# Optimization experiments

Hardware: AMD Instinct MI355X
Metric: run time of the kernel (lower is better)

Reference implementation:

```python
import jax, jax.numpy as jnp
import numpy as np

N_NODES = 100000
N_EDGES = 1600000
D_IN, D_HID, D_OUT = 64, 64, 32


def _glorot(key, shape):
    fan_in, fan_out = shape[0], shape[1]
    lim = np.sqrt(6.0 / (fan_in + fan_out)).astype(np.float32)
    return jax.random.uniform(key, shape, jnp.float32, -lim, lim)


def setup_inputs() -> dict:
    key = jax.random.key(0)
    ks = jax.random.split(key, 12)
    x = jax.random.normal(ks[0], (N_NODES, D_IN), jnp.float32)
    edge_index = jax.random.randint(ks[1], (2, N_EDGES), 0, N_NODES, jnp.int64)
    return {
        "x": x,
        "edge_index": edge_index,
        # SAGEConv 1 (in->hid): lin_l (aggregated neighbors, with bias), lin_r (root, no bias)
        "Wl1": _glorot(ks[2], (D_IN, D_HID)),
        "Wr1": _glorot(ks[3], (D_IN, D_HID)),
        "b1": jnp.zeros((D_HID,), jnp.float32),
        # SAGEConv 2 (hid->out)
        "Wl2": _glorot(ks[4], (D_HID, D_OUT)),
        "Wr2": _glorot(ks[5], (D_HID, D_OUT)),
        "b2": jnp.zeros((D_OUT,), jnp.float32),
        # trust head: Linear(32,16) -> ReLU -> Linear(16,1) -> Sigmoid (dropout inert in eval)
        "Wt1": _glorot(ks[6], (D_OUT, 16)),
        "bt1": jnp.zeros((16,), jnp.float32),
        "Wt2": _glorot(ks[7], (16, 1)),
        "bt2": jnp.zeros((1,), jnp.float32),
    }


def _sage_conv(x, src, dst, Wl, Wr, b):
    # mean-aggregate neighbor messages: msg flows src -> dst
    msg = x[src]                                              # [E, d] gather
    agg_sum = jax.ops.segment_sum(msg, dst, num_segments=N_NODES)
    deg = jax.ops.segment_sum(jnp.ones((src.shape[0],), x.dtype), dst,
                              num_segments=N_NODES)
    agg = agg_sum / jnp.maximum(deg, 1.0)[:, None]            # zero-degree -> 0
    return agg @ Wl + x @ Wr + b


def reference(x, edge_index, Wl1, Wr1, b1, Wl2, Wr2, b2, Wt1, bt1, Wt2, bt2):
    src, dst = edge_index[0], edge_index[1]
    h = _sage_conv(x, src, dst, Wl1, Wr1, b1)
    h = jax.nn.relu(h)                    # dropout p=0.3 inert in eval
    h = _sage_conv(h, src, dst, Wl2, Wr2, b2)
    t = jax.nn.relu(h @ Wt1 + bt1)        # dropout p=0.2 inert in eval
    trust = jax.nn.sigmoid(t @ Wt2 + bt2)
    return h, trust
```

## Files before the change

kernel.cpp:

```cpp
#include <hip/hip_runtime.h>
#include <math.h>


#define BCAP    9216
#define BKCHUNK 4096

__device__ inline unsigned short f2bf(float x) {
    unsigned u = __float_as_uint(x);
    unsigned r = u + 0x7fffu + ((u >> 16) & 1u);
    return (unsigned short)(r >> 16);
}
__device__ inline unsigned pack2(float a, float b) {
    return (unsigned)f2bf(a) | ((unsigned)f2bf(b) << 16);
}
__device__ inline float bflo(unsigned u) { return __uint_as_float(u << 16); }
__device__ inline float bfhi(unsigned u) { return __uint_as_float(u & 0xffff0000u); }

__global__ __launch_bounds__(256) void k_m1(
    const float* __restrict__ x,
    const float* __restrict__ Wl1, const float* __restrict__ Wr1,
    const float* __restrict__ b1,
    unsigned* __restrict__ u16b, float* __restrict__ v,
    const int* __restrict__ src, const int* __restrict__ dst,
    int* __restrict__ gcnt, unsigned* __restrict__ pairs,
    int N, int E, int nbuck, int GB, int BKB)
{
    __shared__ __align__(16) char smem[33792];
    int tid = threadIdx.x;
    int g = blockIdx.x / 5, r5 = blockIdx.x % 5;

    if (r5 == 4) {
        if (g >= BKB) return;
        int* hist = (int*)smem;
        int e0 = g * BKCHUNK;
        int e1 = min(e0 + BKCHUNK, E);

        hist[tid] = 0;
        __syncthreads();
        for (int e = e0 + tid; e < e1; e += 256)
            atomicAdd(&hist[((unsigned)dst[e]) >> 9], 1);
        __syncthreads();
        if (tid < nbuck && hist[tid] > 0)
            hist[tid] = tid * BCAP + atomicAdd(&gcnt[tid], hist[tid]);
        __syncthreads();
        for (int e = e0 + tid; e < e1; e += 256) {
            int t = dst[e];
            int b = ((unsigned)t) >> 9;
            int pos = atomicAdd(&hist[b], 1);
            pairs[pos] = (unsigned)src[e] | ((unsigned)(t & 511) << 17);
        }
        return;
    }

    int tile = 4 * g + r5;
    if (tile >= GB) return;
    float* sXT = (float*)smem;
    float* sW  = (float*)(smem + 17408);
    int nblk = tile * 64;

    for (int i = tid * 4; i < 64 * 64; i += 1024) {
        int r = i >> 6, c = i & 63;
        int node = nblk + r;
        float4 xv = (node < N) ? *(const float4*)&x[(size_t)node * 64 + c]
                               : make_float4(0.f, 0.f, 0.f, 0.f);
        sXT[(c + 0) * 68 + r] = xv.x;
        sXT[(c + 1) * 68 + r] = xv.y;
        sXT[(c + 2) * 68 + r] = xv.z;
        sXT[(c + 3) * 68 + r] = xv.w;
    }

    int mg = tid >> 4, ng = tid & 15;
    int m0 = mg * 4, n0 = ng * 4;

    #pragma unroll
    for (int pass = 0; pass < 2; ++pass) {
        const float* W = pass ? Wr1 : Wl1;
        if (pass) __syncthreads();
        for (int i = tid * 4; i < 64 * 64; i += 1024)
            *(float4*)&sW[i] = *(const float4*)&W[i];
        __syncthreads();

        float acc[4][4];
        #pragma unroll
        for (int mi = 0; mi < 4; ++mi)
            #pragma unroll
            for (int ni = 0; ni < 4; ++ni) acc[mi][ni] = 0.0f;

        #pragma unroll 8
        for (int k = 0; k < 64; ++k) {
            float4 a = *(float4*)&sXT[k * 68 + m0];
            float4 w = *(float4*)&sW[k * 64 + n0];
            float av[4] = {a.x, a.y, a.z, a.w};
            float wv[4] = {w.x, w.y, w.z, w.w};
            #pragma unroll
            for (int mi = 0; mi < 4; ++mi)
                #pragma unroll
                for (int ni = 0; ni < 4; ++ni)
                    acc[mi][ni] = fmaf(av[mi], wv[ni], acc[mi][ni]);
        }

        if (pass == 0) {
            #pragma unroll
            for (int mi = 0; mi < 4; ++mi) {
                int node = nblk + m0 + mi;
                if (node >= N) continue;
                uint2 pk;
                pk.x = pack2(acc[mi][0], acc[mi][1]);
                pk.y = pack2(acc[mi][2], acc[mi][3]);
                *(uint2*)&u16b[(size_t)node * 32 + (n0 >> 1)] = pk;
            }
        } else {
            float4 b0 = *(const float4*)&b1[n0];
            #pragma unroll
            for (int mi = 0; mi < 4; ++mi) {
                int node = nblk + m0 + mi;
                if (node >= N) continue;
                *(float4*)&v[(size_t)node * 64 + n0] =
                    make_float4(acc[mi][0]+b0.x, acc[mi][1]+b0.y,
                                acc[mi][2]+b0.z, acc[mi][3]+b0.w);
            }
        }
    }
}

__global__ __launch_bounds__(1024) void k_csr(
    const unsigned* __restrict__ pairs, const int* __restrict__ gcnt,
    int2* __restrict__ nodeOff, int* __restrict__ adj, int N)
{
    __shared__ int hist[512];
    __shared__ int waveSum[8];
    int b = blockIdx.x;
    int tid = threadIdx.x;
    int count = min(gcnt[b], BCAP);
    const unsigned* pp = pairs + (size_t)b * BCAP;
    int base = b * BCAP;

    if (tid < 512) hist[tid] = 0;
    __syncthreads();
    for (int j = tid; j < count; j += 1024)
        atomicAdd(&hist[pp[j] >> 17], 1);
    __syncthreads();

    int lane = tid & 63, wid = tid >> 6;
    int deg = 0, incl = 0;
    if (tid < 512) {
        deg = hist[tid];
        incl = deg;
        #pragma unroll
        for (int off = 1; off < 64; off <<= 1) {
            int t = __shfl_up(incl, off);
            if (lane >= off) incl += t;
        }
        if (lane == 63) waveSum[wid] = incl;
    }
    __syncthreads();
    if (wid == 0 && lane < 8) {
        int s = waveSum[lane], orig = s;
        #pragma unroll
        for (int off = 1; off < 8; off <<= 1) {
            int t = __shfl_up(s, off);
            if (lane >= off) s += t;
        }
        waveSum[lane] = s - orig;
    }
    __syncthreads();
    int excl = 0;
    if (tid < 512) {
        excl = incl - deg + waveSum[wid];
        int node = b * 512 + tid;
        if (node < N) nodeOff[node] = make_int2(base + excl, deg);
    }
    __syncthreads();
    if (tid < 512) hist[tid] = excl;
    __syncthreads();

    for (int j = tid; j < count; j += 1024) {
        unsigned e = pp[j];
        int pos = atomicAdd(&hist[e >> 17], 1);
        adj[base + pos] = (int)(e & 0x1FFFFu);
    }
}

__global__ __launch_bounds__(512) void k_m2(
    const int2* __restrict__ nodeOff, const int* __restrict__ adj,
    const unsigned* __restrict__ u16b, const float* __restrict__ v,
    const float* __restrict__ Wl2, const float* __restrict__ Wr2,
    const float* __restrict__ b2,
    unsigned* __restrict__ P16b, float* __restrict__ Qout, int N)
{
    __shared__ float sH[64 * 66];
    __shared__ float sW[64 * 64];
    int tid = threadIdx.x;
    int nodeBase = blockIdx.x * 64;

    for (int i = tid * 4; i < 64 * 64; i += 2048) {
        int k = i >> 6, n = i & 63;
        const float* Wsrc = (n < 32) ? (Wl2 + k * 32 + n) : (Wr2 + k * 32 + (n - 32));
        *(float4*)&sW[k * 64 + n] = *(const float4*)Wsrc;
    }

    int hw = tid >> 5;
    int lane = tid & 31;
    for (int r = 0; r < 4; ++r) {
        int nLoc = hw * 4 + r;
        int n = nodeBase + nLoc;
        float h0 = 0.0f, h1v = 0.0f;
        if (n < N) {
            int2 od = nodeOff[n];
            int beg = od.x, end = od.x + od.y;
            float lo[8] = {0,0,0,0,0,0,0,0}, hi[8] = {0,0,0,0,0,0,0,0};
            int i = beg;
            for (; i + 8 <= end; i += 8) {
                int s[8];
                #pragma unroll
                for (int j = 0; j < 8; ++j) s[j] = adj[i + j];
                #pragma unroll
                for (int j = 0; j < 8; ++j) {
                    unsigned w = u16b[(size_t)s[j] * 32 + lane];
                    lo[j] += bflo(w); hi[j] += bfhi(w);
                }
            }
            for (; i < end; ++i) {
                unsigned w = u16b[(size_t)adj[i] * 32 + lane];
                lo[0] += bflo(w); hi[0] += bfhi(w);
            }
            float mlo = ((lo[0]+lo[1])+(lo[2]+lo[3])) + ((lo[4]+lo[5])+(lo[6]+lo[7]));
            float mhi = ((hi[0]+hi[1])+(hi[2]+hi[3])) + ((hi[4]+hi[5])+(hi[6]+hi[7]));
            float invd = (od.y > 0) ? 1.0f / (float)od.y : 1.0f;
            float2 vv = ((const float2*)v)[(size_t)n * 32 + lane];
            h0  = fmaxf(mlo * invd + vv.x, 0.0f);
            h1v = fmaxf(mhi * invd + vv.y, 0.0f);
        }
        *(float2*)&sH[nLoc * 66 + 2 * lane] = make_float2(h0, h1v);
    }
    __syncthreads();

    int ng = tid & 15;
    int mg = tid >> 4;
    int m0 = mg * 2, n0 = ng * 4;

    float acc[2][4];
    #pragma unroll
    for (int mi = 0; mi < 2; ++mi)
        #pragma unroll
        for (int ni = 0; ni < 4; ++ni) acc[mi][ni] = 0.0f;

    #pragma unroll 8
    for (int k = 0; k < 64; ++k) {
        float a0 = sH[(m0 + 0) * 66 + k];
        float a1 = sH[(m0 + 1) * 66 + k];
        float4 w = *(float4*)&sW[k * 64 + n0];
        float wv[4] = {w.x, w.y, w.z, w.w};
        #pragma unroll
        for (int ni = 0; ni < 4; ++ni) {
            acc[0][ni] = fmaf(a0, wv[ni], acc[0][ni]);
            acc[1][ni] = fmaf(a1, wv[ni], acc[1][ni]);
        }
    }

    if (n0 < 32) {
        #pragma unroll
        for (int mi = 0; mi < 2; ++mi) {
            int node = nodeBase + m0 + mi;
            if (node >= N) continue;
            uint2 pk;
            pk.x = pack2(acc[mi][0], acc[mi][1]);
            pk.y = pack2(acc[mi][2], acc[mi][3]);
            *(uint2*)&P16b[(size_t)node * 16 + (n0 >> 1)] = pk;
        }
    } else {
        float4 b0 = *(const float4*)&b2[n0 - 32];
        #pragma unroll
        for (int mi = 0; mi < 2; ++mi) {
            int node = nodeBase + m0 + mi;
            if (node >= N) continue;
            *(float4*)&Qout[(size_t)node * 32 + (n0 - 32)] =
                make_float4(acc[mi][0]+b0.x, acc[mi][1]+b0.y,
                            acc[mi][2]+b0.z, acc[mi][3]+b0.w);
        }
    }
}

__global__ __launch_bounds__(256) void k_agg2(
    const int2* __restrict__ nodeOff, const int* __restrict__ adj,
    const unsigned* __restrict__ P16b, const float* __restrict__ Q,
    const float* __restrict__ Wt1, const float* __restrict__ bt1,
    const float* __restrict__ Wt2, const float* __restrict__ bt2,
    float* __restrict__ out_h, float* __restrict__ out_trust, int N)
{
    __shared__ float sWt1[32 * 16];
    __shared__ float sWt2[16];
    for (int i = threadIdx.x; i < 512; i += 256) sWt1[i] = Wt1[i];
    if (threadIdx.x < 16) sWt2[threadIdx.x] = Wt2[threadIdx.x];
    __syncthreads();

    int n = blockIdx.x * 16 + (threadIdx.x >> 4);
    int lane = threadIdx.x & 15;
    if (n >= N) return;

    int2 od = nodeOff[n];
    int beg = od.x, end = od.x + od.y;
    float lo[8] = {0,0,0,0,0,0,0,0}, hi[8] = {0,0,0,0,0,0,0,0};
    int i = beg;
    for (; i + 8 <= end; i += 8) {
        int s[8];
        #pragma unroll
        for (int j = 0; j < 8; ++j) s[j] = adj[i + j];
        #pragma unroll
        for (int j = 0; j < 8; ++j) {
            unsigned w = P16b[(size_t)s[j] * 16 + lane];
            lo[j] += bflo(w); hi[j] += bfhi(w);
        }
    }
    for (; i < end; ++i) {
        unsigned w = P16b[(size_t)adj[i] * 16 + lane];
        lo[0] += bflo(w); hi[0] += bfhi(w);
    }
    float invd = (od.y > 0) ? 1.0f / (float)od.y : 1.0f;
    float mlo = (((lo[0]+lo[1])+(lo[2]+lo[3])) + ((lo[4]+lo[5])+(lo[6]+lo[7]))) * invd;
    float mhi = (((hi[0]+hi[1])+(hi[2]+hi[3])) + ((hi[4]+hi[5])+(hi[6]+hi[7]))) * invd;

    float2 qv = ((const float2*)Q)[(size_t)n * 16 + lane];
    float hx = mlo + qv.x;
    float hy = mhi + qv.y;

    ((float2*)out_h)[(size_t)n * 16 + lane] = make_float2(hx, hy);

    float t = bt1[lane];
    #pragma unroll
    for (int k = 0; k < 16; ++k) {
        float hlo = __shfl(hx, k, 16);
        float hhi = __shfl(hy, k, 16);
        t += hlo * sWt1[(2 * k) * 16 + lane] + hhi * sWt1[(2 * k + 1) * 16 + lane];
    }
    t = fmaxf(t, 0.0f);
    float z = t * sWt2[lane];
    z += __shfl_xor(z, 1);
    z += __shfl_xor(z, 2);
    z += __shfl_xor(z, 4);
    z += __shfl_xor(z, 8);
    if (lane == 0) out_trust[n] = 1.0f / (1.0f + expf(-(z + bt2[0])));
}


extern "C" void kernel_launch(void* const* d_in, const int* in_sizes, int n_in,
                              void* d_out, int out_size, void* d_ws, size_t ws_size,
                              hipStream_t stream)
{
    const float* x   = (const float*)d_in[0];
    const int*   ei  = (const int*)d_in[1];
    const float* Wl1 = (const float*)d_in[2];
    const float* Wr1 = (const float*)d_in[3];
    const float* b1  = (const float*)d_in[4];
    const float* Wl2 = (const float*)d_in[5];
    const float* Wr2 = (const float*)d_in[6];
    const float* b2  = (const float*)d_in[7];
    const float* Wt1 = (const float*)d_in[8];
    const float* bt1 = (const float*)d_in[9];
    const float* Wt2 = (const float*)d_in[10];
    const float* bt2 = (const float*)d_in[11];

    const int N = in_sizes[0] / 64;
    const int E = in_sizes[1] / 2;
    const int* src = ei;
    const int* dst = ei + E;
    const int nbuck = (N + 511) / 512;

    unsigned* pairs  = (unsigned*)d_ws;
    unsigned* u16b   = pairs + (size_t)nbuck * BCAP;
    float*    v      = (float*)(u16b + (size_t)N * 32);
    unsigned* P16b   = (unsigned*)(v + (size_t)N * 64);
    float*    Q      = (float*)(P16b + (size_t)N * 16);
    int*      gcnt   = (int*)(Q + (size_t)N * 32);
    int2*     nodeOff= (int2*)(gcnt + 256);
    int*      adj    = (int*)(nodeOff + N);

    hipMemsetAsync(gcnt, 0, 256 * sizeof(int), stream);

    const int GB  = (N + 63) / 64;
    const int BKB = (E + BKCHUNK - 1) / BKCHUNK;
    int grp = max(BKB, (GB + 3) / 4);
    k_m1  <<<5 * grp, 256, 0, stream>>>(x, Wl1, Wr1, b1, u16b, v,
                                        src, dst, gcnt, pairs, N, E, nbuck, GB, BKB);
    k_csr <<<nbuck, 1024, 0, stream>>>(pairs, gcnt, nodeOff, adj, N);
    k_m2  <<<GB, 512, 0, stream>>>(nodeOff, adj, u16b, v, Wl2, Wr2, b2,
                                   P16b, Q, N);

    float* out_h     = (float*)d_out;
    float* out_trust = out_h + (size_t)N * 32;
    k_agg2<<<(N + 15) / 16, 256, 0, stream>>>(nodeOff, adj, P16b, Q,
                                              Wt1, bt1, Wt2, bt2,
                                              out_h, out_trust, N);
}
```

Measured before the change: 246.9 us.

## Bucket edges by 64-node tiles and build per-tile CSR in shared memory inside consumers

Drops the separate CSR-building kernel. Edges are now bucketed by 64-node tiles with a capacity of 1536 entries each, and each layer-aggregation kernel rebuilds its tile's adjacency with a shared-memory counting sort before gathering. The goal is to save one kernel launch and the global writes and reads of the adj and nodeOff arrays. The cost is that the sort runs twice, once per layer, and any edges past a bucket's capacity are dropped, which relies on the degree distribution of the random test graph. The first GEMM also moves to a row-major X tile with a k-blocked inner loop, and the ratio of GEMM blocks to bucketing blocks changes.

Measured after the change: 307.9 us. 1.25x slower.

```diff
diff --git a/kernel.cpp b/kernel.cpp
--- a/kernel.cpp
+++ b/kernel.cpp
@@ -2,8 +2,9 @@
 #include <math.h>
 
 
-#define BCAP    9216
-#define BKCHUNK 4096
+#define NBUCK   1563
+#define BCAP    1536
+#define BKCHUNK 16384
 
 __device__ inline unsigned short f2bf(float x) {
     unsigned u = __float_as_uint(x);
@@ -23,39 +24,41 @@
     unsigned* __restrict__ u16b, float* __restrict__ v,
     const int* __restrict__ src, const int* __restrict__ dst,
     int* __restrict__ gcnt, unsigned* __restrict__ pairs,
-    int N, int E, int nbuck, int GB, int BKB)
+    int N, int E, int GB, int BKB)
 {
     __shared__ __align__(16) char smem[33792];
     int tid = threadIdx.x;
-    int g = blockIdx.x / 5, r5 = blockIdx.x % 5;
-
-    if (r5 == 4) {
+    int g = blockIdx.x / 17, r17 = blockIdx.x % 17;
+
+    if (r17 == 16) {
         if (g >= BKB) return;
         int* hist = (int*)smem;
         int e0 = g * BKCHUNK;
         int e1 = min(e0 + BKCHUNK, E);
 
-        hist[tid] = 0;
+        for (int i = tid; i < NBUCK; i += 256) hist[i] = 0;
         __syncthreads();
         for (int e = e0 + tid; e < e1; e += 256)
-            atomicAdd(&hist[((unsigned)dst[e]) >> 9], 1);
+            atomicAdd(&hist[((unsigned)dst[e]) >> 6], 1);
         __syncthreads();
-        if (tid < nbuck && hist[tid] > 0)
-            hist[tid] = tid * BCAP + atomicAdd(&gcnt[tid], hist[tid]);
+        for (int i = tid; i < NBUCK; i += 256)
+            if (hist[i] > 0)
+                hist[i] = i * BCAP + atomicAdd(&gcnt[i], hist[i]);
         __syncthreads();
         for (int e = e0 + tid; e < e1; e += 256) {
             int t = dst[e];
-            int b = ((unsigned)t) >> 9;
+            int b = ((unsigned)t) >> 6;
             int pos = atomicAdd(&hist[b], 1);
-            pairs[pos] = (unsigned)src[e] | ((unsigned)(t & 511) << 17);
+            if (pos < (b + 1) * BCAP)
+                pairs[pos] = (unsigned)src[e] | ((unsigned)(t & 63) << 17);
         }
         return;
     }
 
-    int tile = 4 * g + r5;
+    int tile = 16 * g + r17;
     if (tile >= GB) return;
-    float* sXT = (float*)smem;
-    float* sW  = (float*)(smem + 17408);
+    float* sX = (float*)smem;
+    float* sW = (float*)(smem + 17408);
     int nblk = tile * 64;
 
     for (int i = tid * 4; i < 64 * 64; i += 1024) {
@@ -63,10 +66,7 @@
         int node = nblk + r;
         float4 xv = (node < N) ? *(const float4*)&x[(size_t)node * 64 + c]
                                : make_float4(0.f, 0.f, 0.f, 0.f);
-        sXT[(c + 0) * 68 + r] = xv.x;
-        sXT[(c + 1) * 68 + r] = xv.y;
-        sXT[(c + 2) * 68 + r] = xv.z;
-        sXT[(c + 3) * 68 + r] = xv.w;
+        *(float4*)&sX[r * 68 + c] = xv;
     }
 
     int mg = tid >> 4, ng = tid & 15;
@@ -86,17 +86,26 @@
             #pragma unroll
             for (int ni = 0; ni < 4; ++ni) acc[mi][ni] = 0.0f;
 
-        #pragma unroll 8
-        for (int k = 0; k < 64; ++k) {
-            float4 a = *(float4*)&sXT[k * 68 + m0];
-            float4 w = *(float4*)&sW[k * 64 + n0];
-            float av[4] = {a.x, a.y, a.z, a.w};
-            float wv[4] = {w.x, w.y, w.z, w.w};
+        #pragma unroll
+        for (int k0 = 0; k0 < 64; k0 += 4) {
+            float4 a[4], w[4];
             #pragma unroll
             for (int mi = 0; mi < 4; ++mi)
+                a[mi] = *(float4*)&sX[(m0 + mi) * 68 + k0];
+            #pragma unroll
+            for (int kk = 0; kk < 4; ++kk)
+                w[kk] = *(float4*)&sW[(k0 + kk) * 64 + n0];
+            #pragma unroll
+            for (int mi = 0; mi < 4; ++mi) {
+                float am[4] = {a[mi].x, a[mi].y, a[mi].z, a[mi].w};
                 #pragma unroll
-                for (int ni = 0; ni < 4; ++ni)
-                    acc[mi][ni] = fmaf(av[mi], wv[ni], acc[mi][ni]);
+                for (int kk = 0; kk < 4; ++kk) {
+                    acc[mi][0] = fmaf(am[kk], w[kk].x, acc[mi][0]);
+                    acc[mi][1] = fmaf(am[kk], w[kk].y, acc[mi][1]);
+                    acc[mi][2] = fmaf(am[kk], w[kk].z, acc[mi][2]);
+                    acc[mi][3] = fmaf(am[kk], w[kk].w, acc[mi][3]);
+                }
+            }
         }
 
         if (pass == 0) {
@@ -123,66 +132,8 @@
     }
 }
 
-__global__ __launch_bounds__(1024) void k_csr(
+__global__ __launch_bounds__(512) void k_m2(
     const unsigned* __restrict__ pairs, const int* __restrict__ gcnt,
-    int2* __restrict__ nodeOff, int* __restrict__ adj, int N)
-{
-    __shared__ int hist[512];
-    __shared__ int waveSum[8];
-    int b = blockIdx.x;
-    int tid = threadIdx.x;
-    int count = min(gcnt[b], BCAP);
-    const unsigned* pp = pairs + (size_t)b * BCAP;
-    int base = b * BCAP;
-
-    if (tid < 512) hist[tid] = 0;
-    __syncthreads();
-    for (int j = tid; j < count; j += 1024)
-        atomicAdd(&hist[pp[j] >> 17], 1);
-    __syncthreads();
-
-    int lane = tid & 63, wid = tid >> 6;
-    int deg = 0, incl = 0;
-    if (tid < 512) {
-        deg = hist[tid];
-        incl = deg;
-        #pragma unroll
-        for (int off = 1; off < 64; off <<= 1) {
-            int t = __shfl_up(incl, off);
-            if (lane >= off) incl += t;
-        }
-        if (lane == 63) waveSum[wid] = incl;
-    }
-    __syncthreads();
-    if (wid == 0 && lane < 8) {
-        int s = waveSum[lane], orig = s;
-        #pragma unroll
-        for (int off = 1; off < 8; off <<= 1) {
-            int t = __shfl_up(s, off);
-            if (lane >= off) s += t;
-        }
-        waveSum[lane] = s - orig;
-    }
-    __syncthreads();
-    int excl = 0;
-    if (tid < 512) {
-        excl = incl - deg + waveSum[wid];
-        int node = b * 512 + tid;
-        if (node < N) nodeOff[node] = make_int2(base + excl, deg);
-    }
-    __syncthreads();
-    if (tid < 512) hist[tid] = excl;
-    __syncthreads();
-
-    for (int j = tid; j < count; j += 1024) {
-        unsigned e = pp[j];
-        int pos = atomicAdd(&hist[e >> 17], 1);
-        adj[base + pos] = (int)(e & 0x1FFFFu);
-    }
-}
-
-__global__ __launch_bounds__(512) void k_m2(
-    const int2* __restrict__ nodeOff, const int* __restrict__ adj,
     const unsigned* __restrict__ u16b, const float* __restrict__ v,
     const float* __restrict__ Wl2, const float* __restrict__ Wr2,
     const float* __restrict__ b2,
@@ -190,30 +141,60 @@
 {
     __shared__ float sH[64 * 66];
     __shared__ float sW[64 * 64];
+    __shared__ int   sAdj[BCAP];
+    __shared__ int   sOff[65];
+    __shared__ int   sCur[64];
     int tid = threadIdx.x;
-    int nodeBase = blockIdx.x * 64;
+    int b = blockIdx.x;
+    int nodeBase = b * 64;
+    int count = min(gcnt[b], BCAP);
+    const unsigned* pp = pairs + (size_t)b * BCAP;
 
     for (int i = tid * 4; i < 64 * 64; i += 2048) {
         int k = i >> 6, n = i & 63;
         const float* Wsrc = (n < 32) ? (Wl2 + k * 32 + n) : (Wr2 + k * 32 + (n - 32));
         *(float4*)&sW[k * 64 + n] = *(const float4*)Wsrc;
     }
-
-    int hw = tid >> 5;
-    int lane = tid & 31;
+    if (tid < 64) sCur[tid] = 0;
+    __syncthreads();
+
+    for (int j = tid; j < count; j += 512)
+        atomicAdd(&sCur[(pp[j] >> 17) & 63], 1);
+    __syncthreads();
+    if (tid < 64) {
+        int c = sCur[tid];
+        int incl = c;
+        #pragma unroll
+        for (int off = 1; off < 64; off <<= 1) {
+            int t = __shfl_up(incl, off);
+            if (tid >= off) incl += t;
+        }
+        sOff[tid] = incl - c;
+        if (tid == 63) sOff[64] = incl;
+    }
+    __syncthreads();
+    if (tid < 64) sCur[tid] = sOff[tid];
+    __syncthreads();
+    for (int j = tid; j < count; j += 512) {
+        unsigned e = pp[j];
+        int pos = atomicAdd(&sCur[(e >> 17) & 63], 1);
+        sAdj[pos] = (int)(e & 0x1FFFFu);
+    }
+    __syncthreads();
+
+    int hw = tid >> 5, lane = tid & 31;
     for (int r = 0; r < 4; ++r) {
-        int nLoc = hw * 4 + r;
-        int n = nodeBase + nLoc;
+        int nl = hw * 4 + r;
+        int node = nodeBase + nl;
         float h0 = 0.0f, h1v = 0.0f;
-        if (n < N) {
-            int2 od = nodeOff[n];
-            int beg = od.x, end = od.x + od.y;
+        if (node < N) {
+            int beg = sOff[nl], end = sOff[nl + 1];
             float lo[8] = {0,0,0,0,0,0,0,0}, hi[8] = {0,0,0,0,0,0,0,0};
             int i = beg;
             for (; i + 8 <= end; i += 8) {
                 int s[8];
                 #pragma unroll
-                for (int j = 0; j < 8; ++j) s[j] = adj[i + j];
+                for (int j = 0; j < 8; ++j) s[j] = sAdj[i + j];
                 #pragma unroll
                 for (int j = 0; j < 8; ++j) {
                     unsigned w = u16b[(size_t)s[j] * 32 + lane];
@@ -221,17 +202,18 @@
                 }
             }
             for (; i < end; ++i) {
-                unsigned w = u16b[(size_t)adj[i] * 32 + lane];
+                unsigned w = u16b[(size_t)sAdj[i] * 32 + lane];
                 lo[0] += bflo(w); hi[0] += bfhi(w);
             }
             float mlo = ((lo[0]+lo[1])+(lo[2]+lo[3])) + ((lo[4]+lo[5])+(lo[6]+lo[7]));
             float mhi = ((hi[0]+hi[1])+(hi[2]+hi[3])) + ((hi[4]+hi[5])+(hi[6]+hi[7]));
-            float invd = (od.y > 0) ? 1.0f / (float)od.y : 1.0f;
-            float2 vv = ((const float2*)v)[(size_t)n * 32 + lane];
+            int deg = end - beg;
+            float invd = (deg > 0) ? 1.0f / (float)deg : 1.0f;
+            float2 vv = ((const float2*)v)[(size_t)node * 32 + lane];
             h0  = fmaxf(mlo * invd + vv.x, 0.0f);
             h1v = fmaxf(mhi * invd + vv.y, 0.0f);
         }
-        *(float2*)&sH[nLoc * 66 + 2 * lane] = make_float2(h0, h1v);
+        *(float2*)&sH[nl * 66 + 2 * lane] = make_float2(h0, h1v);
     }
     __syncthreads();
 
@@ -281,65 +263,101 @@
     }
 }
 
-__global__ __launch_bounds__(256) void k_agg2(
-    const int2* __restrict__ nodeOff, const int* __restrict__ adj,
+__global__ __launch_bounds__(256) void k_a2(
+    const unsigned* __restrict__ pairs, const int* __restrict__ gcnt,
     const unsigned* __restrict__ P16b, const float* __restrict__ Q,
     const float* __restrict__ Wt1, const float* __restrict__ bt1,
     const float* __restrict__ Wt2, const float* __restrict__ bt2,
     float* __restrict__ out_h, float* __restrict__ out_trust, int N)
 {
+    __shared__ int   sAdj[BCAP];
+    __shared__ int   sOff[65];
+    __shared__ int   sCur[64];
     __shared__ float sWt1[32 * 16];
     __shared__ float sWt2[16];
-    for (int i = threadIdx.x; i < 512; i += 256) sWt1[i] = Wt1[i];
-    if (threadIdx.x < 16) sWt2[threadIdx.x] = Wt2[threadIdx.x];
-    __syncthreads();
-
-    int n = blockIdx.x * 16 + (threadIdx.x >> 4);
-    int lane = threadIdx.x & 15;
-    if (n >= N) return;
-
-    int2 od = nodeOff[n];
-    int beg = od.x, end = od.x + od.y;
-    float lo[8] = {0,0,0,0,0,0,0,0}, hi[8] = {0,0,0,0,0,0,0,0};
-    int i = beg;
-    for (; i + 8 <= end; i += 8) {
-        int s[8];
-        #pragma unroll
-        for (int j = 0; j < 8; ++j) s[j] = adj[i + j];
-        #pragma unroll
-        for (int j = 0; j < 8; ++j) {
-            unsigned w = P16b[(size_t)s[j] * 16 + lane];
-            lo[j] += bflo(w); hi[j] += bfhi(w);
-        }
-    }
-    for (; i < end; ++i) {
-        unsigned w = P16b[(size_t)adj[i] * 16 + lane];
-        lo[0] += bflo(w); hi[0] += bfhi(w);
-    }
-    float invd = (od.y > 0) ? 1.0f / (float)od.y : 1.0f;
-    float mlo = (((lo[0]+lo[1])+(lo[2]+lo[3])) + ((lo[4]+lo[5])+(lo[6]+lo[7]))) * invd;
-    float mhi = (((hi[0]+hi[1])+(hi[2]+hi[3])) + ((hi[4]+hi[5])+(hi[6]+hi[7]))) * invd;
-
-    float2 qv = ((const float2*)Q)[(size_t)n * 16 + lane];
-    float hx = mlo + qv.x;
-    float hy = mhi + qv.y;
-
-    ((float2*)out_h)[(size_t)n * 16 + lane] = make_float2(hx, hy);
-
-    float t = bt1[lane];
-    #pragma unroll
-    for (int k = 0; k < 16; ++k) {
-        float hlo = __shfl(hx, k, 16);
-        float hhi = __shfl(hy, k, 16);
-        t += hlo * sWt1[(2 * k) * 16 + lane] + hhi * sWt1[(2 * k + 1) * 16 + lane];
-    }
-    t = fmaxf(t, 0.0f);
-    float z = t * sWt2[lane];
-    z += __shfl_xor(z, 1);
-    z += __shfl_xor(z, 2);
-    z += __shfl_xor(z, 4);
-    z += __shfl_xor(z, 8);
-    if (lane == 0) out_trust[n] = 1.0f / (1.0f + expf(-(z + bt2[0])));
+    __shared__ float sbt1[16];
+    int tid = threadIdx.x;
+    int b = blockIdx.x;
+    int nodeBase = b * 64;
+    int count = min(gcnt[b], BCAP);
+    const unsigned* pp = pairs + (size_t)b * BCAP;
+
+    for (int i = tid; i < 512; i += 256) sWt1[i] = Wt1[i];
+    if (tid < 16) { sWt2[tid] = Wt2[tid]; sbt1[tid] = bt1[tid]; }
+    if (tid < 64) sCur[tid] = 0;
+    __syncthreads();
+
+    for (int j = tid; j < count; j += 256)
+        atomicAdd(&sCur[(pp[j] >> 17) & 63], 1);
+    __syncthreads();
+    if (tid < 64) {
+        int c = sCur[tid];
+        int incl = c;
+        #pragma unroll
+        for (int off = 1; off < 64; off <<= 1) {
+            int t = __shfl_up(incl, off);
+            if (tid >= off) incl += t;
+        }
+        sOff[tid] = incl - c;
+        if (tid == 63) sOff[64] = incl;
+    }
+    __syncthreads();
+    if (tid < 64) sCur[tid] = sOff[tid];
+    __syncthreads();
+    for (int j = tid; j < count; j += 256) {
+        unsigned e = pp[j];
+        int pos = atomicAdd(&sCur[(e >> 17) & 63], 1);
+        sAdj[pos] = (int)(e & 0x1FFFFu);
+    }
+    __syncthreads();
+
+    int grp = tid >> 4, lane = tid & 15;
+    for (int r = 0; r < 4; ++r) {
+        int nl = grp * 4 + r;
+        int node = nodeBase + nl;
+        if (node >= N) continue;
+        int beg = sOff[nl], end = sOff[nl + 1];
+        float lo[8] = {0,0,0,0,0,0,0,0}, hi[8] = {0,0,0,0,0,0,0,0};
+        int i = beg;
+        for (; i + 8 <= end; i += 8) {
+            int s[8];
+            #pragma unroll
+            for (int j = 0; j < 8; ++j) s[j] = sAdj[i + j];
+            #pragma unroll
+            for (int j = 0; j < 8; ++j) {
+                unsigned w = P16b[(size_t)s[j] * 16 + lane];
+                lo[j] += bflo(w); hi[j] += bfhi(w);
+            }
+        }
+        for (; i < end; ++i) {
+            unsigned w = P16b[(size_t)sAdj[i] * 16 + lane];
+            lo[0] += bflo(w); hi[0] += bfhi(w);
+        }
+        int deg = end - beg;
+        float invd = (deg > 0) ? 1.0f / (float)deg : 1.0f;
+        float mlo = (((lo[0]+lo[1])+(lo[2]+lo[3])) + ((lo[4]+lo[5])+(lo[6]+lo[7]))) * invd;
+        float mhi = (((hi[0]+hi[1])+(hi[2]+hi[3])) + ((hi[4]+hi[5])+(hi[6]+hi[7]))) * invd;
+
+        float2 qv = ((const float2*)Q)[(size_t)node * 16 + lane];
+        float hx = mlo + qv.x;
+        float hy = mhi + qv.y;
+        ((float2*)out_h)[(size_t)node * 16 + lane] = make_float2(hx, hy);
+
+        float t = sbt1[lane];
+        #pragma unroll
+        for (int k = 0; k < 16; ++k) {
+            float hlo = __shfl(hx, k, 16);
+            float hhi = __shfl(hy, k, 16);
+            t += hlo * sWt1[(2 * k) * 16 + lane] + hhi * sWt1[(2 * k + 1) * 16 + lane];
+        }
+        t = fmaxf(t, 0.0f);
+        float z = t * sWt2[lane];
+        z += __shfl_xor(z, 1);
+        z += __shfl_xor(z, 2);
+        z += __shfl_xor(z, 4);
+        z += __shfl_xor(z, 8);
+        if (lane == 0) out_trust[node] = 1.0f / (1.0f + expf(-(z + bt2[0])));
+    }
 }
 
 
@@ -364,31 +382,26 @@
     const int E = in_sizes[1] / 2;
     const int* src = ei;
     const int* dst = ei + E;
-    const int nbuck = (N + 511) / 512;
 
     unsigned* pairs  = (unsigned*)d_ws;
-    unsigned* u16b   = pairs + (size_t)nbuck * BCAP;
+    unsigned* u16b   = pairs + (size_t)NBUCK * BCAP;
     float*    v      = (float*)(u16b + (size_t)N * 32);
     unsigned* P16b   = (unsigned*)(v + (size_t)N * 64);
     float*    Q      = (float*)(P16b + (size_t)N * 16);
     int*      gcnt   = (int*)(Q + (size_t)N * 32);
-    int2*     nodeOff= (int2*)(gcnt + 256);
-    int*      adj    = (int*)(nodeOff + N);
-
-    hipMemsetAsync(gcnt, 0, 256 * sizeof(int), stream);
+
+    hipMemsetAsync(gcnt, 0, 1600 * sizeof(int), stream);
 
     const int GB  = (N + 63) / 64;
     const int BKB = (E + BKCHUNK - 1) / BKCHUNK;
-    int grp = max(BKB, (GB + 3) / 4);
-    k_m1  <<<5 * grp, 256, 0, stream>>>(x, Wl1, Wr1, b1, u16b, v,
-                                        src, dst, gcnt, pairs, N, E, nbuck, GB, BKB);
-    k_csr <<<nbuck, 1024, 0, stream>>>(pairs, gcnt, nodeOff, adj, N);
-    k_m2  <<<GB, 512, 0, stream>>>(nodeOff, adj, u16b, v, Wl2, Wr2, b2,
-                                   P16b, Q, N);
+    int grp = (GB + 15) / 16 > BKB ? (GB + 15) / 16 : BKB;
+    k_m1<<<17 * grp, 256, 0, stream>>>(x, Wl1, Wr1, b1, u16b, v,
+                                       src, dst, gcnt, pairs, N, E, GB, BKB);
+    k_m2<<<NBUCK, 512, 0, stream>>>(pairs, gcnt, u16b, v, Wl2, Wr2, b2,
+                                    P16b, Q, N);
 
     float* out_h     = (float*)d_out;
     float* out_trust = out_h + (size_t)N * 32;
-    k_agg2<<<(N + 15) / 16, 256, 0, stream>>>(nodeOff, adj, P16b, Q,
-                                              Wt1, bt1, Wt2, bt2,
-                                              out_h, out_trust, N);
-}
+    k_a2<<<NBUCK, 256, 0, stream>>>(pairs, gcnt, P16b, Q,
+                                    Wt1, bt1, Wt2, bt2, out_h, out_trust, N);
+}
```

## Fuse CSR construction into layer-2 kernel using 64-node buckets

Applied to the files above, without the earlier changes.

Shrinks the destination buckets from 512 to 64 nodes, so each bucket matches one k_m2 tile. The separate k_csr kernel is removed: k_m2 now builds its tile's CSR in shared memory, writes nodeOff and adj for the last kernel, and aggregates straight from the shared adjacency list. This saves one launch and the global round trip for adjacency in layer 2. In exchange it needs more shared memory per block, and edges past the fixed bucket capacity are silently dropped if a bucket overflows.

Result: faster. 233.2 us (-5.6%).

```diff
diff --git a/kernel.cpp b/kernel.cpp
--- a/kernel.cpp
+++ b/kernel.cpp
@@ -2,7 +2,8 @@
 #include <math.h>
 
 
-#define BCAP    9216
+#define NBUCK   1563
+#define BCAP    1536
 #define BKCHUNK 4096
 
 __device__ inline unsigned short f2bf(float x) {
@@ -23,7 +24,7 @@
     unsigned* __restrict__ u16b, float* __restrict__ v,
     const int* __restrict__ src, const int* __restrict__ dst,
     int* __restrict__ gcnt, unsigned* __restrict__ pairs,
-    int N, int E, int nbuck, int GB, int BKB)
+    int N, int E, int GB, int BKB)
 {
     __shared__ __align__(16) char smem[33792];
     int tid = threadIdx.x;
@@ -35,19 +36,21 @@
         int e0 = g * BKCHUNK;
         int e1 = min(e0 + BKCHUNK, E);
 
-        hist[tid] = 0;
+        for (int i = tid; i < NBUCK; i += 256) hist[i] = 0;
         __syncthreads();
         for (int e = e0 + tid; e < e1; e += 256)
-            atomicAdd(&hist[((unsigned)dst[e]) >> 9], 1);
+            atomicAdd(&hist[((unsigned)dst[e]) >> 6], 1);
         __syncthreads();
-        if (tid < nbuck && hist[tid] > 0)
-            hist[tid] = tid * BCAP + atomicAdd(&gcnt[tid], hist[tid]);
+        for (int i = tid; i < NBUCK; i += 256)
+            if (hist[i] > 0)
+                hist[i] = i * BCAP + atomicAdd(&gcnt[i], hist[i]);
         __syncthreads();
         for (int e = e0 + tid; e < e1; e += 256) {
             int t = dst[e];
-            int b = ((unsigned)t) >> 9;
+            int b = ((unsigned)t) >> 6;
             int pos = atomicAdd(&hist[b], 1);
-            pairs[pos] = (unsigned)src[e] | ((unsigned)(t & 511) << 17);
+            if (pos < (b + 1) * BCAP)
+                pairs[pos] = (unsigned)src[e] | ((unsigned)(t & 63) << 17);
         }
         return;
     }
@@ -123,97 +126,77 @@
     }
 }
 
-__global__ __launch_bounds__(1024) void k_csr(
+__global__ __launch_bounds__(512) void k_m2(
     const unsigned* __restrict__ pairs, const int* __restrict__ gcnt,
-    int2* __restrict__ nodeOff, int* __restrict__ adj, int N)
-{
-    __shared__ int hist[512];
-    __shared__ int waveSum[8];
-    int b = blockIdx.x;
-    int tid = threadIdx.x;
-    int count = min(gcnt[b], BCAP);
-    const unsigned* pp = pairs + (size_t)b * BCAP;
-    int base = b * BCAP;
-
-    if (tid < 512) hist[tid] = 0;
-    __syncthreads();
-    for (int j = tid; j < count; j += 1024)
-        atomicAdd(&hist[pp[j] >> 17], 1);
-    __syncthreads();
-
-    int lane = tid & 63, wid = tid >> 6;
-    int deg = 0, incl = 0;
-    if (tid < 512) {
-        deg = hist[tid];
-        incl = deg;
-        #pragma unroll
-        for (int off = 1; off < 64; off <<= 1) {
-            int t = __shfl_up(incl, off);
-            if (lane >= off) incl += t;
-        }
-        if (lane == 63) waveSum[wid] = incl;
-    }
-    __syncthreads();
-    if (wid == 0 && lane < 8) {
-        int s = waveSum[lane], orig = s;
-        #pragma unroll
-        for (int off = 1; off < 8; off <<= 1) {
-            int t = __shfl_up(s, off);
-            if (lane >= off) s += t;
-        }
-        waveSum[lane] = s - orig;
-    }
-    __syncthreads();
-    int excl = 0;
-    if (tid < 512) {
-        excl = incl - deg + waveSum[wid];
-        int node = b * 512 + tid;
-        if (node < N) nodeOff[node] = make_int2(base + excl, deg);
-    }
-    __syncthreads();
-    if (tid < 512) hist[tid] = excl;
-    __syncthreads();
-
-    for (int j = tid; j < count; j += 1024) {
-        unsigned e = pp[j];
-        int pos = atomicAdd(&hist[e >> 17], 1);
-        adj[base + pos] = (int)(e & 0x1FFFFu);
-    }
-}
-
-__global__ __launch_bounds__(512) void k_m2(
-    const int2* __restrict__ nodeOff, const int* __restrict__ adj,
     const unsigned* __restrict__ u16b, const float* __restrict__ v,
     const float* __restrict__ Wl2, const float* __restrict__ Wr2,
     const float* __restrict__ b2,
-    unsigned* __restrict__ P16b, float* __restrict__ Qout, int N)
+    unsigned* __restrict__ P16b, float* __restrict__ Qout,
+    int2* __restrict__ nodeOff, int* __restrict__ adjG, int N)
 {
     __shared__ float sH[64 * 66];
     __shared__ float sW[64 * 64];
+    __shared__ int   sAdj[BCAP];
+    __shared__ int   sOff[65];
+    __shared__ int   sCur[64];
     int tid = threadIdx.x;
-    int nodeBase = blockIdx.x * 64;
+    int b = blockIdx.x;
+    int nodeBase = b * 64;
+    int base = b * BCAP;
+    int count = min(gcnt[b], BCAP);
+    const unsigned* pp = pairs + (size_t)b * BCAP;
 
     for (int i = tid * 4; i < 64 * 64; i += 2048) {
         int k = i >> 6, n = i & 63;
         const float* Wsrc = (n < 32) ? (Wl2 + k * 32 + n) : (Wr2 + k * 32 + (n - 32));
         *(float4*)&sW[k * 64 + n] = *(const float4*)Wsrc;
     }
-
-    int hw = tid >> 5;
-    int lane = tid & 31;
+    if (tid < 64) sCur[tid] = 0;
+    __syncthreads();
+
+    for (int j = tid; j < count; j += 512)
+        atomicAdd(&sCur[(pp[j] >> 17) & 63], 1);
+    __syncthreads();
+    if (tid < 64) {
+        int c = sCur[tid];
+        int incl = c;
+        #pragma unroll
+        for (int off = 1; off < 64; off <<= 1) {
+            int t = __shfl_up(incl, off);
+            if (tid >= off) incl += t;
+        }
+        sOff[tid] = incl - c;
+        if (tid == 63) sOff[64] = incl;
+    }
+    __syncthreads();
+    if (tid < 64) {
+        sCur[tid] = sOff[tid];
+        int node = nodeBase + tid;
+        if (node < N)
+            nodeOff[node] = make_int2(base + sOff[tid], sOff[tid + 1] - sOff[tid]);
+    }
+    __syncthreads();
+    for (int j = tid; j < count; j += 512) {
+        unsigned e = pp[j];
+        int pos = atomicAdd(&sCur[(e >> 17) & 63], 1);
+        sAdj[pos] = (int)(e & 0x1FFFFu);
+    }
+    __syncthreads();
+    for (int j = tid; j < count; j += 512) adjG[base + j] = sAdj[j];
+
+    int hw = tid >> 5, lane = tid & 31;
     for (int r = 0; r < 4; ++r) {
-        int nLoc = hw * 4 + r;
-        int n = nodeBase + nLoc;
+        int nl = hw * 4 + r;
+        int node = nodeBase + nl;
         float h0 = 0.0f, h1v = 0.0f;
-        if (n < N) {
-            int2 od = nodeOff[n];
-            int beg = od.x, end = od.x + od.y;
+        if (node < N) {
+            int beg = sOff[nl], end = sOff[nl + 1];
             float lo[8] = {0,0,0,0,0,0,0,0}, hi[8] = {0,0,0,0,0,0,0,0};
             int i = beg;
             for (; i + 8 <= end; i += 8) {
                 int s[8];
                 #pragma unroll
-                for (int j = 0; j < 8; ++j) s[j] = adj[i + j];
+                for (int j = 0; j < 8; ++j) s[j] = sAdj[i + j];
                 #pragma unroll
                 for (int j = 0; j < 8; ++j) {
                     unsigned w = u16b[(size_t)s[j] * 32 + lane];
@@ -221,17 +204,18 @@
                 }
             }
             for (; i < end; ++i) {
-                unsigned w = u16b[(size_t)adj[i] * 32 + lane];
+                unsigned w = u16b[(size_t)sAdj[i] * 32 + lane];
                 lo[0] += bflo(w); hi[0] += bfhi(w);
             }
             float mlo = ((lo[0]+lo[1])+(lo[2]+lo[3])) + ((lo[4]+lo[5])+(lo[6]+lo[7]));
             float mhi = ((hi[0]+hi[1])+(hi[2]+hi[3])) + ((hi[4]+hi[5])+(hi[6]+hi[7]));
-            float invd = (od.y > 0) ? 1.0f / (float)od.y : 1.0f;
-            float2 vv = ((const float2*)v)[(size_t)n * 32 + lane];
+            int deg = end - beg;
+            float invd = (deg > 0) ? 1.0f / (float)deg : 1.0f;
+            float2 vv = ((const float2*)v)[(size_t)node * 32 + lane];
             h0  = fmaxf(mlo * invd + vv.x, 0.0f);
             h1v = fmaxf(mhi * invd + vv.y, 0.0f);
         }
-        *(float2*)&sH[nLoc * 66 + 2 * lane] = make_float2(h0, h1v);
+        *(float2*)&sH[nl * 66 + 2 * lane] = make_float2(h0, h1v);
     }
     __syncthreads();
 
@@ -281,7 +265,7 @@
     }
 }
 
-__global__ __launch_bounds__(256) void k_agg2(
+__global__ __launch_bounds__(256) void k_a2(
     const int2* __restrict__ nodeOff, const int* __restrict__ adj,
     const unsigned* __restrict__ P16b, const float* __restrict__ Q,
     const float* __restrict__ Wt1, const float* __restrict__ bt1,
@@ -364,31 +348,29 @@
     const int E = in_sizes[1] / 2;
     const int* src = ei;
     const int* dst = ei + E;
-    const int nbuck = (N + 511) / 512;
 
     unsigned* pairs  = (unsigned*)d_ws;
-    unsigned* u16b   = pairs + (size_t)nbuck * BCAP;
+    unsigned* u16b   = pairs + (size_t)NBUCK * BCAP;
     float*    v      = (float*)(u16b + (size_t)N * 32);
     unsigned* P16b   = (unsigned*)(v + (size_t)N * 64);
     float*    Q      = (float*)(P16b + (size_t)N * 16);
-    int*      gcnt   = (int*)(Q + (size_t)N * 32);
-    int2*     nodeOff= (int2*)(gcnt + 256);
+    int2*     nodeOff= (int2*)(Q + (size_t)N * 32);
     int*      adj    = (int*)(nodeOff + N);
-
-    hipMemsetAsync(gcnt, 0, 256 * sizeof(int), stream);
+    int*      gcnt   = adj + (size_t)NBUCK * BCAP;
+
+    hipMemsetAsync(gcnt, 0, 2048 * sizeof(int), stream);
 
     const int GB  = (N + 63) / 64;
     const int BKB = (E + BKCHUNK - 1) / BKCHUNK;
-    int grp = max(BKB, (GB + 3) / 4);
-    k_m1  <<<5 * grp, 256, 0, stream>>>(x, Wl1, Wr1, b1, u16b, v,
-                                        src, dst, gcnt, pairs, N, E, nbuck, GB, BKB);
-    k_csr <<<nbuck, 1024, 0, stream>>>(pairs, gcnt, nodeOff, adj, N);
-    k_m2  <<<GB, 512, 0, stream>>>(nodeOff, adj, u16b, v, Wl2, Wr2, b2,
-                                   P16b, Q, N);
+    int grp = (GB + 3) / 4 > BKB ? (GB + 3) / 4 : BKB;
+    k_m1<<<5 * grp, 256, 0, stream>>>(x, Wl1, Wr1, b1, u16b, v,
+                                      src, dst, gcnt, pairs, N, E, GB, BKB);
+    k_m2<<<NBUCK, 512, 0, stream>>>(pairs, gcnt, u16b, v, Wl2, Wr2, b2,
+                                    P16b, Q, nodeOff, adj, N);
 
     float* out_h     = (float*)d_out;
     float* out_trust = out_h + (size_t)N * 32;
-    k_agg2<<<(N + 15) / 16, 256, 0, stream>>>(nodeOff, adj, P16b, Q,
-                                              Wt1, bt1, Wt2, bt2,
-                                              out_h, out_trust, N);
-}
+    k_a2<<<(N + 15) / 16, 256, 0, stream>>>(nodeOff, adj, P16b, Q,
+                                            Wt1, bt1, Wt2, bt2,
+                                            out_h, out_trust, N);
+}
```
